# Kernel tuning notes

Hardware: AMD Instinct MI355X
Metric: run time of the kernel (lower is better)

The kernel has to match this reference:

```python
import jax, jax.numpy as jnp
import numpy as np

CAPACITY = 1024


def setup_inputs() -> dict:
    T, H, I, E, K = 2048, 1024, 1408, 8, 2
    key = jax.random.key(0)
    k0, k1, k2, k3, k4 = jax.random.split(key, 5)
    hidden_states = jax.random.normal(k0, (T, H), dtype=jnp.float32)
    w1 = jax.random.normal(k1, (E, 2 * I, H), dtype=jnp.float32) * 0.02  # [gate; up]
    w2 = jax.random.normal(k2, (E, H, I), dtype=jnp.float32) * 0.02
    topk_weights = jax.random.uniform(k3, (T, K), dtype=jnp.float32)
    topk_ids = jax.random.randint(k4, (T, K), 0, E, dtype=jnp.int32)
    return {"hidden_states": hidden_states, "w1": w1, "w2": w2,
            "topk_weights": topk_weights, "topk_ids": topk_ids}


def reference(hidden_states, w1, w2, topk_weights, topk_ids):
    # MoE: prepare(dispatch) -> grouped expert GEMM (silu-gated MLP) -> finalize(combine)
    T, H = hidden_states.shape
    E = w1.shape[0]
    I = w2.shape[2]
    K = topk_ids.shape[1]
    C = CAPACITY

    # ---- prepare: dispatch token copies to per-expert buffers ----
    flat_ids = topk_ids.reshape(-1)                       # (T*K,)
    onehot = jax.nn.one_hot(flat_ids, E, dtype=jnp.int32)  # (T*K, E)
    cs = jnp.cumsum(onehot, axis=0)                        # running per-expert counts
    pos = jnp.take_along_axis(cs, flat_ids[:, None], axis=1)[:, 0] - 1  # slot in expert buffer
    keep = pos < C
    pos_c = jnp.where(keep, pos, 0)

    x_flat = jnp.repeat(hidden_states, K, axis=0)          # (T*K, H)
    x_e = jnp.zeros((E, C, H), dtype=hidden_states.dtype)
    x_e = x_e.at[flat_ids, pos_c].add(jnp.where(keep[:, None], x_flat, 0.0))

    # ---- grouped expert GEMM: silu(gate) * up, then down-proj ----
    h = jnp.einsum('ech,eoh->eco', x_e, w1)                # (E, C, 2I)
    gate, up = h[..., :I], h[..., I:]
    act = jax.nn.silu(gate) * up                           # (E, C, I)
    y = jnp.einsum('eci,ehi->ech', act, w2)                # (E, C, H)

    # ---- finalize: gather back, apply router weights, reduce over top-k ----
    y_flat = y[flat_ids, pos_c] * (keep[:, None].astype(y.dtype)) \
             * topk_weights.reshape(-1, 1)                 # (T*K, H)
    out = y_flat.reshape(T, K, H).sum(axis=1)              # (T, H)
    return out.astype(hidden_states.dtype)
```

## Files before the change

kernel.cpp:

```cpp
#include <hip/hip_runtime.h>

#define NE 8
#define CAP 1024
#define HD 1024
#define ID 1408
#define TT 2048

typedef __attribute__((ext_vector_type(8))) short bf16x8;
typedef __attribute__((ext_vector_type(4))) float f32x4;
typedef unsigned short u16;
typedef unsigned int u32;
typedef unsigned long long u64;

__device__ __forceinline__ u16 f2bf(float f) {
  u32 u = __float_as_uint(f);
  u = (u + 0x7fffu + ((u >> 16) & 1u)) >> 16;
  return (u16)u;
}

__device__ __forceinline__ bf16x8 pack8(float4 a, float4 b) {
  bf16x8 r;
  r[0] = (short)f2bf(a.x); r[1] = (short)f2bf(a.y);
  r[2] = (short)f2bf(a.z); r[3] = (short)f2bf(a.w);
  r[4] = (short)f2bf(b.x); r[5] = (short)f2bf(b.y);
  r[6] = (short)f2bf(b.z); r[7] = (short)f2bf(b.w);
  return r;
}

__device__ __forceinline__ void async_cp16(const void* g, void* l) {
  __builtin_amdgcn_global_load_lds(
      (const __attribute__((address_space(1))) u32*)g,
      (__attribute__((address_space(3))) u32*)l, 16, 0, 0);
}

#define W1B (NE * 2 * ID / 4)
#define W2B (NE * HD * ID / 4096)
#define XB (TT * HD / 4096)
__global__ __launch_bounds__(256) void prep_kernel(
    const float4* __restrict__ w1, bf16x8* __restrict__ bw1,
    const float4* __restrict__ w2, bf16x8* __restrict__ bw2,
    const float4* __restrict__ x, bf16x8* __restrict__ bx,
    float4* __restrict__ out, const int* __restrict__ ids,
    int* __restrict__ rowmap, int* __restrict__ counts) {
  int b = blockIdx.x;
  int tid = threadIdx.x;
  if (b == 0) {
    __shared__ unsigned char ids_s[TT * 2];
    __shared__ int sc[256][NE + 1];
    for (int i = tid; i < TT * 2; i += 256) ids_s[i] = (unsigned char)ids[i];
    __syncthreads();
    int base = tid * 16;
    u64 own64 = 0;
#pragma unroll
    for (int j = 0; j < 16; ++j) own64 += 1ull << (ids_s[base + j] * 8);
    int own[NE];
#pragma unroll
    for (int e = 0; e < NE; ++e) {
      own[e] = (int)((own64 >> (e * 8)) & 0xff);
      sc[tid][e] = own[e];
    }
    __syncthreads();
    for (int off = 1; off < 256; off <<= 1) {
      int v[NE];
      if (tid >= off) {
#pragma unroll
        for (int e = 0; e < NE; ++e) v[e] = sc[tid - off][e];
      }
      __syncthreads();
      if (tid >= off) {
#pragma unroll
        for (int e = 0; e < NE; ++e) sc[tid][e] += v[e];
      }
      __syncthreads();
    }
    if (tid == 255) {
#pragma unroll
      for (int e = 0; e < NE; ++e) counts[e] = sc[255][e] < CAP ? sc[255][e] : CAP;
    }
    int excl[NE];
#pragma unroll
    for (int e = 0; e < NE; ++e) excl[e] = sc[tid][e] - own[e];
    __syncthreads();
#pragma unroll
    for (int e = 0; e < NE; ++e) sc[tid][e] = excl[e];
#pragma unroll
    for (int j = 0; j < 16; ++j) {
      int f = base + j;
      int e = ids_s[f];
      int p = sc[tid][e]++;
      if (p < CAP) rowmap[e * CAP + p] = f;
    }
    return;
  }
  int bb = b - 1;
  if (bb < W1B) {
    int rl = tid >> 6, c = tid & 63;
    int g = bb * 4 + rl;
    int e = g / (2 * ID);
    int n = g - e * (2 * ID);
    int j = (n < ID) ? n : (n - ID);
    int np = (j >> 4) * 32 + (j & 15) + ((n < ID) ? 0 : 16);
    const float4* src = w1 + ((size_t)e * 2 * ID + n) * (HD / 4);
    bf16x8* dst = bw1 + ((size_t)e * 2 * ID + np) * (HD / 8);
    float4 v0 = src[c * 2];
    float4 v1 = src[c * 2 + 1];
    float4 v2 = src[128 + c * 2];
    float4 v3 = src[128 + c * 2 + 1];
    dst[c] = pack8(v0, v1);
    dst[64 + c] = pack8(v2, v3);
  } else if (bb < W1B + W2B) {
    size_t base4 = (size_t)(bb - W1B) * 1024;
    float4 v0 = w2[base4 + tid * 2];
    float4 v1 = w2[base4 + tid * 2 + 1];
    float4 v2 = w2[base4 + 512 + tid * 2];
    float4 v3 = w2[base4 + 512 + tid * 2 + 1];
    bf16x8* dst = bw2 + base4 / 2;
    dst[tid] = pack8(v0, v1);
    dst[256 + tid] = pack8(v2, v3);
  } else {
    size_t base4 = (size_t)(bb - W1B - W2B) * 1024;
    float4 v0 = x[base4 + tid * 2];
    float4 v1 = x[base4 + tid * 2 + 1];
    float4 v2 = x[base4 + 512 + tid * 2];
    float4 v3 = x[base4 + 512 + tid * 2 + 1];
    bf16x8* dst = bx + base4 / 2;
    dst[tid] = pack8(v0, v1);
    dst[256 + tid] = pack8(v2, v3);
    float4 z = {0.f, 0.f, 0.f, 0.f};
    out[base4 + tid] = z;
    out[base4 + 256 + tid] = z;
    out[base4 + 512 + tid] = z;
    out[base4 + 768 + tid] = z;
  }
}

__global__ __launch_bounds__(256) void gemm1_kernel(
    const u16* __restrict__ A, const u16* __restrict__ B, u16* __restrict__ Hb,
    const int* __restrict__ rowmap, const int* __restrict__ counts) {
  int e = blockIdx.x;
  int count = counts[e];
  int m0 = blockIdx.y * 128;
  if (m0 >= count) return;
  int n0 = blockIdx.z * 128;
  int tid = threadIdx.x;
  int lane = tid & 63, wid = tid >> 6;
  int wm = wid >> 1, wn = wid & 1;
  int q = lane >> 4, lm = lane & 15;

  __shared__ __align__(16) char sm[32768];
  char* smA = sm;
  char* smB = sm + 16384;

  int rloc = tid >> 3;
  int chs = ((tid & 7) ^ (rloc & 7)) * 8;
  const u16* aP[4];
  const u16* bP[4];
#pragma unroll
  for (int i = 0; i < 4; ++i) {
    int gr = m0 + rloc + 32 * i;
    int f = (gr < count) ? rowmap[e * CAP + gr] : 0;
    aP[i] = A + (size_t)(f >> 1) * HD + chs;
    bP[i] = B + ((size_t)e * 2 * ID + n0 + rloc + 32 * i) * HD + chs;
  }

  f32x4 zero = {0.f, 0.f, 0.f, 0.f};
  f32x4 acc[4][4];
#pragma unroll
  for (int mi = 0; mi < 4; ++mi)
#pragma unroll
    for (int ni = 0; ni < 4; ++ni) acc[mi][ni] = zero;

  for (int kt = 0; kt < HD / 64; ++kt) {
    int ko = kt * 64;
#pragma unroll
    for (int i = 0; i < 4; ++i)
      async_cp16(aP[i] + ko, smA + (i * 256 + tid) * 16);
#pragma unroll
    for (int i = 0; i < 4; ++i)
      async_cp16(bP[i] + ko, smB + (i * 256 + tid) * 16);
    asm volatile("s_waitcnt vmcnt(0)" ::: "memory");
    __syncthreads();
#pragma unroll
    for (int s = 0; s < 2; ++s) {
      bf16x8 af[4], bfr[4];
#pragma unroll
      for (int mi = 0; mi < 4; ++mi) {
        int row = wm * 64 + mi * 16 + lm;
        af[mi] = *(const bf16x8*)(smA + row * 128 + (((s * 4 + q) ^ (lm & 7)) * 16));
      }
#pragma unroll
      for (int ni = 0; ni < 4; ++ni) {
        int row = wn * 64 + ni * 16 + lm;
        bfr[ni] = *(const bf16x8*)(smB + row * 128 + (((s * 4 + q) ^ (lm & 7)) * 16));
      }
#pragma unroll
      for (int mi = 0; mi < 4; ++mi)
#pragma unroll
        for (int ni = 0; ni < 4; ++ni)
          acc[mi][ni] = __builtin_amdgcn_mfma_f32_16x16x32_bf16(af[mi], bfr[ni], acc[mi][ni], 0, 0, 0);
    }
    __syncthreads();
  }

  u16* smOut = (u16*)sm;
#pragma unroll
  for (int mi = 0; mi < 4; ++mi) {
#pragma unroll
    for (int k = 0; k < 2; ++k) {
      int colL = wn * 32 + k * 16 + lm;
#pragma unroll
      for (int r = 0; r < 4; ++r) {
        float g = acc[mi][2 * k][r];
        float u = acc[mi][2 * k + 1][r];
        float a = g / (1.f + __expf(-g)) * u;
        int row = wm * 64 + mi * 16 + q * 4 + r;
        smOut[row * 72 + colL] = f2bf(a);
      }
    }
  }
  __syncthreads();
  {
    int row = tid >> 1, seg = tid & 1;
    const u16* sp = smOut + row * 72 + seg * 32;
    bf16x8 v0 = *(const bf16x8*)sp;
    bf16x8 v1 = *(const bf16x8*)(sp + 8);
    bf16x8 v2 = *(const bf16x8*)(sp + 16);
    bf16x8 v3 = *(const bf16x8*)(sp + 24);
    u16* dp = Hb + ((size_t)e * CAP + m0 + row) * ID + (n0 >> 1) + seg * 32;
    *(bf16x8*)dp = v0;
    *(bf16x8*)(dp + 8) = v1;
    *(bf16x8*)(dp + 16) = v2;
    *(bf16x8*)(dp + 24) = v3;
  }
}

__global__ __launch_bounds__(256) void gemm2_kernel(
    const u16* __restrict__ A, const u16* __restrict__ B, float* __restrict__ out,
    const int* __restrict__ rowmap, const int* __restrict__ counts,
    const float* __restrict__ tw) {
  int e = blockIdx.x;
  int count = counts[e];
  int m0 = blockIdx.y * 64;
  if (m0 >= count) return;
  int n0 = blockIdx.z * 64;
  int tid = threadIdx.x;
  int lane = tid & 63, wid = tid >> 6;
  int wm = wid >> 1, wn = wid & 1;
  int q = lane >> 4, lm = lane & 15;

  __shared__ __align__(16) char smA[64 * 128];
  __shared__ __align__(16) char smB[64 * 128];

  int rloc = tid >> 3;
  int chs = ((tid & 7) ^ (rloc & 7)) * 8;
  const u16* aP[2];
  const u16* bP[2];
#pragma unroll
  for (int i = 0; i < 2; ++i) {
    aP[i] = A + ((size_t)e * CAP + m0 + rloc + 32 * i) * ID + chs;
    bP[i] = B + ((size_t)e * HD + n0 + rloc + 32 * i) * ID + chs;
  }

  f32x4 zero = {0.f, 0.f, 0.f, 0.f};
  f32x4 acc[2][2];
#pragma unroll
  for (int mi = 0; mi < 2; ++mi)
#pragma unroll
    for (int ni = 0; ni < 2; ++ni) acc[mi][ni] = zero;

  for (int kt = 0; kt < ID / 64; ++kt) {
    int ko = kt * 64;
#pragma unroll
    for (int i = 0; i < 2; ++i) {
      async_cp16(aP[i] + ko, smA + (i * 256 + tid) * 16);
      async_cp16(bP[i] + ko, smB + (i * 256 + tid) * 16);
    }
    asm volatile("s_waitcnt vmcnt(0)" ::: "memory");
    __syncthreads();
#pragma unroll
    for (int s = 0; s < 2; ++s) {
      bf16x8 af[2], bfr[2];
#pragma unroll
      for (int mi = 0; mi < 2; ++mi) {
        int row = wm * 32 + mi * 16 + lm;
        af[mi] = *(const bf16x8*)(smA + row * 128 + (((s * 4 + q) ^ (lm & 7)) * 16));
      }
#pragma unroll
      for (int ni = 0; ni < 2; ++ni) {
        int row = wn * 32 + ni * 16 + lm;
        bfr[ni] = *(const bf16x8*)(smB + row * 128 + (((s * 4 + q) ^ (lm & 7)) * 16));
      }
#pragma unroll
      for (int mi = 0; mi < 2; ++mi)
#pragma unroll
        for (int ni = 0; ni < 2; ++ni)
          acc[mi][ni] = __builtin_amdgcn_mfma_f32_16x16x32_bf16(af[mi], bfr[ni], acc[mi][ni], 0, 0, 0);
    }
    __syncthreads();
  }

#pragma unroll
  for (int mi = 0; mi < 2; ++mi) {
#pragma unroll
    for (int r = 0; r < 4; ++r) {
      int grow = m0 + wm * 32 + mi * 16 + q * 4 + r;
      if (grow < count) {
        int f = rowmap[e * CAP + grow];
        float w = tw[f];
        int t = f >> 1;
#pragma unroll
        for (int ni = 0; ni < 2; ++ni) {
          int col = n0 + wn * 32 + ni * 16 + lm;
          atomicAdd(&out[(size_t)t * HD + col], w * acc[mi][ni][r]);
        }
      }
    }
  }
}

extern "C" void kernel_launch(void* const* d_in, const int* in_sizes, int n_in,
                              void* d_out, int out_size, void* d_ws, size_t ws_size,
                              hipStream_t stream) {
  const float* hidden = (const float*)d_in[0];
  const float* w1 = (const float*)d_in[1];
  const float* w2 = (const float*)d_in[2];
  const float* tw = (const float*)d_in[3];
  const int* ids = (const int*)d_in[4];
  float* out = (float*)d_out;

  char* p = (char*)d_ws;
  auto alloc = [&](size_t b) { char* r = p; p += (b + 255) & ~(size_t)255; return r; };
  u16* bw1 = (u16*)alloc((size_t)NE * 2 * ID * HD * 2);
  u16* bw2 = (u16*)alloc((size_t)NE * HD * ID * 2);
  u16* bx = (u16*)alloc((size_t)TT * HD * 2);
  u16* hbuf = (u16*)alloc((size_t)NE * CAP * ID * 2);
  int* rowmap = (int*)alloc((size_t)NE * CAP * 4);
  int* counts = (int*)alloc((size_t)NE * 4);

  prep_kernel<<<1 + W1B + W2B + XB, 256, 0, stream>>>(
      (const float4*)w1, (bf16x8*)bw1, (const float4*)w2, (bf16x8*)bw2,
      (const float4*)hidden, (bf16x8*)bx, (float4*)out, ids, rowmap, counts);

  gemm1_kernel<<<dim3(NE, CAP / 128, 2 * ID / 128), 256, 0, stream>>>(
      bx, bw1, hbuf, rowmap, counts);

  gemm2_kernel<<<dim3(NE, CAP / 64, HD / 64), 256, 0, stream>>>(
      hbuf, bw2, out, rowmap, counts, tw);
}
```

Baseline: 272.5 us.

## Double-buffer LDS in expert GEMMs, persistent M loop, larger gemm2 tile

Both expert GEMM kernels now double-buffer shared memory, issuing the next K-tile's async copies before computing on the current one. The grid's M dimension is cut to 4 blocks that stride over rows in steps of 512, so fewer blocks exit early. gemm2 grows its tile from 64x64 to 128x64, and the MFMA sections are wrapped in s_setprio. Shared memory per block doubles, which may lower occupancy, and the strided loop can unbalance work when per-expert counts differ.

```diff
diff --git a/kernel.cpp b/kernel.cpp
--- a/kernel.cpp
+++ b/kernel.cpp
@@ -139,98 +139,116 @@
     const int* __restrict__ rowmap, const int* __restrict__ counts) {
   int e = blockIdx.x;
   int count = counts[e];
-  int m0 = blockIdx.y * 128;
-  if (m0 >= count) return;
   int n0 = blockIdx.z * 128;
   int tid = threadIdx.x;
   int lane = tid & 63, wid = tid >> 6;
   int wm = wid >> 1, wn = wid & 1;
   int q = lane >> 4, lm = lane & 15;
 
-  __shared__ __align__(16) char sm[32768];
-  char* smA = sm;
-  char* smB = sm + 16384;
+  __shared__ __align__(16) char sm[2][32768];
 
   int rloc = tid >> 3;
   int chs = ((tid & 7) ^ (rloc & 7)) * 8;
-  const u16* aP[4];
+  int ar = (wm * 64 + lm) * 128;
+  int br = 16384 + (wn * 64 + lm) * 128;
+  int cs0 = (q ^ (lm & 7)) * 16;
+  int cs1 = ((4 + q) ^ (lm & 7)) * 16;
+
   const u16* bP[4];
 #pragma unroll
-  for (int i = 0; i < 4; ++i) {
-    int gr = m0 + rloc + 32 * i;
-    int f = (gr < count) ? rowmap[e * CAP + gr] : 0;
-    aP[i] = A + (size_t)(f >> 1) * HD + chs;
+  for (int i = 0; i < 4; ++i)
     bP[i] = B + ((size_t)e * 2 * ID + n0 + rloc + 32 * i) * HD + chs;
-  }
-
-  f32x4 zero = {0.f, 0.f, 0.f, 0.f};
-  f32x4 acc[4][4];
-#pragma unroll
-  for (int mi = 0; mi < 4; ++mi)
-#pragma unroll
-    for (int ni = 0; ni < 4; ++ni) acc[mi][ni] = zero;
-
-  for (int kt = 0; kt < HD / 64; ++kt) {
-    int ko = kt * 64;
-#pragma unroll
-    for (int i = 0; i < 4; ++i)
-      async_cp16(aP[i] + ko, smA + (i * 256 + tid) * 16);
-#pragma unroll
-    for (int i = 0; i < 4; ++i)
-      async_cp16(bP[i] + ko, smB + (i * 256 + tid) * 16);
+
+  for (int m0 = blockIdx.y * 128; m0 < count; m0 += 512) {
+    const u16* aP[4];
+#pragma unroll
+    for (int i = 0; i < 4; ++i) {
+      int gr = m0 + rloc + 32 * i;
+      int f = (gr < count) ? rowmap[e * CAP + gr] : 0;
+      aP[i] = A + (size_t)(f >> 1) * HD + chs;
+    }
+
+    f32x4 zero = {0.f, 0.f, 0.f, 0.f};
+    f32x4 acc[4][4];
+#pragma unroll
+    for (int mi = 0; mi < 4; ++mi)
+#pragma unroll
+      for (int ni = 0; ni < 4; ++ni) acc[mi][ni] = zero;
+
+#define STAGE1(buf, kt)                                                    \
+  do {                                                                     \
+    int ko_ = (kt) * 64;                                                   \
+    async_cp16(aP[0] + ko_, sm[buf] + (0 * 256 + tid) * 16);               \
+    async_cp16(aP[1] + ko_, sm[buf] + (1 * 256 + tid) * 16);               \
+    async_cp16(aP[2] + ko_, sm[buf] + (2 * 256 + tid) * 16);               \
+    async_cp16(aP[3] + ko_, sm[buf] + (3 * 256 + tid) * 16);               \
+    async_cp16(bP[0] + ko_, sm[buf] + 16384 + (0 * 256 + tid) * 16);       \
+    async_cp16(bP[1] + ko_, sm[buf] + 16384 + (1 * 256 + tid) * 16);       \
+    async_cp16(bP[2] + ko_, sm[buf] + 16384 + (2 * 256 + tid) * 16);       \
+    async_cp16(bP[3] + ko_, sm[buf] + 16384 + (3 * 256 + tid) * 16);       \
+  } while (0)
+
+    STAGE1(0, 0);
     asm volatile("s_waitcnt vmcnt(0)" ::: "memory");
     __syncthreads();
-#pragma unroll
-    for (int s = 0; s < 2; ++s) {
-      bf16x8 af[4], bfr[4];
-#pragma unroll
-      for (int mi = 0; mi < 4; ++mi) {
-        int row = wm * 64 + mi * 16 + lm;
-        af[mi] = *(const bf16x8*)(smA + row * 128 + (((s * 4 + q) ^ (lm & 7)) * 16));
-      }
-#pragma unroll
-      for (int ni = 0; ni < 4; ++ni) {
-        int row = wn * 64 + ni * 16 + lm;
-        bfr[ni] = *(const bf16x8*)(smB + row * 128 + (((s * 4 + q) ^ (lm & 7)) * 16));
-      }
-#pragma unroll
-      for (int mi = 0; mi < 4; ++mi)
+    int cur = 0;
+    for (int kt = 0; kt < HD / 64; ++kt) {
+      if (kt < HD / 64 - 1) STAGE1(cur ^ 1, kt + 1);
+      const char* sb = sm[cur];
+#pragma unroll
+      for (int s = 0; s < 2; ++s) {
+        int cs = s ? cs1 : cs0;
+        bf16x8 af[4], bfr[4];
+#pragma unroll
+        for (int mi = 0; mi < 4; ++mi)
+          af[mi] = *(const bf16x8*)(sb + ar + mi * 2048 + cs);
 #pragma unroll
         for (int ni = 0; ni < 4; ++ni)
-          acc[mi][ni] = __builtin_amdgcn_mfma_f32_16x16x32_bf16(af[mi], bfr[ni], acc[mi][ni], 0, 0, 0);
-    }
-    __syncthreads();
-  }
-
-  u16* smOut = (u16*)sm;
-#pragma unroll
-  for (int mi = 0; mi < 4; ++mi) {
-#pragma unroll
-    for (int k = 0; k < 2; ++k) {
-      int colL = wn * 32 + k * 16 + lm;
-#pragma unroll
-      for (int r = 0; r < 4; ++r) {
-        float g = acc[mi][2 * k][r];
-        float u = acc[mi][2 * k + 1][r];
-        float a = g / (1.f + __expf(-g)) * u;
-        int row = wm * 64 + mi * 16 + q * 4 + r;
-        smOut[row * 72 + colL] = f2bf(a);
-      }
-    }
-  }
-  __syncthreads();
-  {
-    int row = tid >> 1, seg = tid & 1;
-    const u16* sp = smOut + row * 72 + seg * 32;
-    bf16x8 v0 = *(const bf16x8*)sp;
-    bf16x8 v1 = *(const bf16x8*)(sp + 8);
-    bf16x8 v2 = *(const bf16x8*)(sp + 16);
-    bf16x8 v3 = *(const bf16x8*)(sp + 24);
-    u16* dp = Hb + ((size_t)e * CAP + m0 + row) * ID + (n0 >> 1) + seg * 32;
-    *(bf16x8*)dp = v0;
-    *(bf16x8*)(dp + 8) = v1;
-    *(bf16x8*)(dp + 16) = v2;
-    *(bf16x8*)(dp + 24) = v3;
+          bfr[ni] = *(const bf16x8*)(sb + br + ni * 2048 + cs);
+        __builtin_amdgcn_s_setprio(1);
+#pragma unroll
+        for (int mi = 0; mi < 4; ++mi)
+#pragma unroll
+          for (int ni = 0; ni < 4; ++ni)
+            acc[mi][ni] = __builtin_amdgcn_mfma_f32_16x16x32_bf16(af[mi], bfr[ni], acc[mi][ni], 0, 0, 0);
+        __builtin_amdgcn_s_setprio(0);
+      }
+      asm volatile("s_waitcnt vmcnt(0)" ::: "memory");
+      __syncthreads();
+      cur ^= 1;
+    }
+
+    u16* smOut = (u16*)sm;
+#pragma unroll
+    for (int mi = 0; mi < 4; ++mi) {
+#pragma unroll
+      for (int k = 0; k < 2; ++k) {
+        int colL = wn * 32 + k * 16 + lm;
+#pragma unroll
+        for (int r = 0; r < 4; ++r) {
+          float g = acc[mi][2 * k][r];
+          float u = acc[mi][2 * k + 1][r];
+          float a = g / (1.f + __expf(-g)) * u;
+          int row = wm * 64 + mi * 16 + q * 4 + r;
+          smOut[row * 72 + colL] = f2bf(a);
+        }
+      }
+    }
+    __syncthreads();
+    {
+      int row = tid >> 1, seg = tid & 1;
+      const u16* sp = smOut + row * 72 + seg * 32;
+      bf16x8 v0 = *(const bf16x8*)sp;
+      bf16x8 v1 = *(const bf16x8*)(sp + 8);
+      bf16x8 v2 = *(const bf16x8*)(sp + 16);
+      bf16x8 v3 = *(const bf16x8*)(sp + 24);
+      u16* dp = Hb + ((size_t)e * CAP + m0 + row) * ID + (n0 >> 1) + seg * 32;
+      *(bf16x8*)dp = v0;
+      *(bf16x8*)(dp + 8) = v1;
+      *(bf16x8*)(dp + 16) = v2;
+      *(bf16x8*)(dp + 24) = v3;
+    }
+    __syncthreads();
   }
 }
 
@@ -240,78 +258,94 @@
     const float* __restrict__ tw) {
   int e = blockIdx.x;
   int count = counts[e];
-  int m0 = blockIdx.y * 64;
-  if (m0 >= count) return;
   int n0 = blockIdx.z * 64;
   int tid = threadIdx.x;
   int lane = tid & 63, wid = tid >> 6;
   int wm = wid >> 1, wn = wid & 1;
   int q = lane >> 4, lm = lane & 15;
 
-  __shared__ __align__(16) char smA[64 * 128];
-  __shared__ __align__(16) char smB[64 * 128];
+  __shared__ __align__(16) char sm[2][24576];
 
   int rloc = tid >> 3;
   int chs = ((tid & 7) ^ (rloc & 7)) * 8;
-  const u16* aP[2];
+  int ar = (wm * 64 + lm) * 128;
+  int br = 16384 + (wn * 32 + lm) * 128;
+  int cs0 = (q ^ (lm & 7)) * 16;
+  int cs1 = ((4 + q) ^ (lm & 7)) * 16;
+
   const u16* bP[2];
 #pragma unroll
-  for (int i = 0; i < 2; ++i) {
-    aP[i] = A + ((size_t)e * CAP + m0 + rloc + 32 * i) * ID + chs;
+  for (int i = 0; i < 2; ++i)
     bP[i] = B + ((size_t)e * HD + n0 + rloc + 32 * i) * ID + chs;
-  }
-
-  f32x4 zero = {0.f, 0.f, 0.f, 0.f};
-  f32x4 acc[2][2];
-#pragma unroll
-  for (int mi = 0; mi < 2; ++mi)
-#pragma unroll
-    for (int ni = 0; ni < 2; ++ni) acc[mi][ni] = zero;
-
-  for (int kt = 0; kt < ID / 64; ++kt) {
-    int ko = kt * 64;
-#pragma unroll
-    for (int i = 0; i < 2; ++i) {
-      async_cp16(aP[i] + ko, smA + (i * 256 + tid) * 16);
-      async_cp16(bP[i] + ko, smB + (i * 256 + tid) * 16);
-    }
+
+  for (int m0 = blockIdx.y * 128; m0 < count; m0 += 512) {
+    const u16* aP[4];
+#pragma unroll
+    for (int i = 0; i < 4; ++i)
+      aP[i] = A + ((size_t)e * CAP + m0 + rloc + 32 * i) * ID + chs;
+
+    f32x4 zero = {0.f, 0.f, 0.f, 0.f};
+    f32x4 acc[4][2];
+#pragma unroll
+    for (int mi = 0; mi < 4; ++mi)
+#pragma unroll
+      for (int ni = 0; ni < 2; ++ni) acc[mi][ni] = zero;
+
+#define STAGE2(buf, kt)                                                    \
+  do {                                                                     \
+    int ko_ = (kt) * 64;                                                   \
+    async_cp16(aP[0] + ko_, sm[buf] + (0 * 256 + tid) * 16);               \
+    async_cp16(aP[1] + ko_, sm[buf] + (1 * 256 + tid) * 16);               \
+    async_cp16(aP[2] + ko_, sm[buf] + (2 * 256 + tid) * 16);               \
+    async_cp16(aP[3] + ko_, sm[buf] + (3 * 256 + tid) * 16);               \
+    async_cp16(bP[0] + ko_, sm[buf] + 16384 + (0 * 256 + tid) * 16);       \
+    async_cp16(bP[1] + ko_, sm[buf] + 16384 + (1 * 256 + tid) * 16);       \
+  } while (0)
+
+    STAGE2(0, 0);
     asm volatile("s_waitcnt vmcnt(0)" ::: "memory");
     __syncthreads();
-#pragma unroll
-    for (int s = 0; s < 2; ++s) {
-      bf16x8 af[2], bfr[2];
-#pragma unroll
-      for (int mi = 0; mi < 2; ++mi) {
-        int row = wm * 32 + mi * 16 + lm;
-        af[mi] = *(const bf16x8*)(smA + row * 128 + (((s * 4 + q) ^ (lm & 7)) * 16));
-      }
-#pragma unroll
-      for (int ni = 0; ni < 2; ++ni) {
-        int row = wn * 32 + ni * 16 + lm;
-        bfr[ni] = *(const bf16x8*)(smB + row * 128 + (((s * 4 + q) ^ (lm & 7)) * 16));
-      }
-#pragma unroll
-      for (int mi = 0; mi < 2; ++mi)
+    int cur = 0;
+    for (int kt = 0; kt < ID / 64; ++kt) {
+      if (kt < ID / 64 - 1) STAGE2(cur ^ 1, kt + 1);
+      const char* sb = sm[cur];
+#pragma unroll
+      for (int s = 0; s < 2; ++s) {
+        int cs = s ? cs1 : cs0;
+        bf16x8 af[4], bfr[2];
+#pragma unroll
+        for (int mi = 0; mi < 4; ++mi)
+          af[mi] = *(const bf16x8*)(sb + ar + mi * 2048 + cs);
 #pragma unroll
         for (int ni = 0; ni < 2; ++ni)
-          acc[mi][ni] = __builtin_amdgcn_mfma_f32_16x16x32_bf16(af[mi], bfr[ni], acc[mi][ni], 0, 0, 0);
-    }
-    __syncthreads();
-  }
-
-#pragma unroll
-  for (int mi = 0; mi < 2; ++mi) {
-#pragma unroll
-    for (int r = 0; r < 4; ++r) {
-      int grow = m0 + wm * 32 + mi * 16 + q * 4 + r;
-      if (grow < count) {
-        int f = rowmap[e * CAP + grow];
-        float w = tw[f];
-        int t = f >> 1;
-#pragma unroll
-        for (int ni = 0; ni < 2; ++ni) {
-          int col = n0 + wn * 32 + ni * 16 + lm;
-          atomicAdd(&out[(size_t)t * HD + col], w * acc[mi][ni][r]);
+          bfr[ni] = *(const bf16x8*)(sb + br + ni * 2048 + cs);
+        __builtin_amdgcn_s_setprio(1);
+#pragma unroll
+        for (int mi = 0; mi < 4; ++mi)
+#pragma unroll
+          for (int ni = 0; ni < 2; ++ni)
+            acc[mi][ni] = __builtin_amdgcn_mfma_f32_16x16x32_bf16(af[mi], bfr[ni], acc[mi][ni], 0, 0, 0);
+        __builtin_amdgcn_s_setprio(0);
+      }
+      asm volatile("s_waitcnt vmcnt(0)" ::: "memory");
+      __syncthreads();
+      cur ^= 1;
+    }
+
+#pragma unroll
+    for (int mi = 0; mi < 4; ++mi) {
+#pragma unroll
+      for (int r = 0; r < 4; ++r) {
+        int grow = m0 + wm * 64 + mi * 16 + q * 4 + r;
+        if (grow < count) {
+          int f = rowmap[e * CAP + grow];
+          float w = tw[f];
+          int t = f >> 1;
+#pragma unroll
+          for (int ni = 0; ni < 2; ++ni) {
+            int col = n0 + wn * 32 + ni * 16 + lm;
+            atomicAdd(&out[(size_t)t * HD + col], w * acc[mi][ni][r]);
+          }
         }
       }
     }
@@ -341,9 +375,9 @@
       (const float4*)w1, (bf16x8*)bw1, (const float4*)w2, (bf16x8*)bw2,
       (const float4*)hidden, (bf16x8*)bx, (float4*)out, ids, rowmap, counts);
 
-  gemm1_kernel<<<dim3(NE, CAP / 128, 2 * ID / 128), 256, 0, stream>>>(
+  gemm1_kernel<<<dim3(NE, 4, 2 * ID / 128), 256, 0, stream>>>(
       bx, bw1, hbuf, rowmap, counts);
 
-  gemm2_kernel<<<dim3(NE, CAP / 64, HD / 64), 256, 0, stream>>>(
+  gemm2_kernel<<<dim3(NE, 4, HD / 64), 256, 0, stream>>>(
       hbuf, bw2, out, rowmap, counts, tw);
 }
```

Result: slower. 296.7 us (+8.9%).

## Triple-buffer async loads in both expert GEMMs and halve gemm1 M tile

Applied to the files above, without the earlier changes.

Both GEMM kernels now keep three shared-memory stages, prefetching two k-tiles ahead and waiting with partial vmcnt counts, so global-to-LDS copies overlap the MFMA work instead of stalling on every iteration. gemm1's M tile shrinks from 128 to 64 rows, which doubles the grid and reduces wasted work on partially filled expert buffers. MFMA sections are wrapped in s_setprio. The trade-off is more LDS per block (72KB in gemm1), which may limit occupancy, and less B-tile reuse in gemm1.

```diff
diff --git a/kernel.cpp b/kernel.cpp
--- a/kernel.cpp
+++ b/kernel.cpp
@@ -134,12 +134,13 @@
   }
 }
 
+#define G1BUF 24576
 __global__ __launch_bounds__(256) void gemm1_kernel(
     const u16* __restrict__ A, const u16* __restrict__ B, u16* __restrict__ Hb,
     const int* __restrict__ rowmap, const int* __restrict__ counts) {
   int e = blockIdx.x;
   int count = counts[e];
-  int m0 = blockIdx.y * 128;
+  int m0 = blockIdx.y * 64;
   if (m0 >= count) return;
   int n0 = blockIdx.z * 128;
   int tid = threadIdx.x;
@@ -147,64 +148,77 @@
   int wm = wid >> 1, wn = wid & 1;
   int q = lane >> 4, lm = lane & 15;
 
-  __shared__ __align__(16) char sm[32768];
-  char* smA = sm;
-  char* smB = sm + 16384;
+  __shared__ __align__(16) char sm[3 * G1BUF];
 
   int rloc = tid >> 3;
   int chs = ((tid & 7) ^ (rloc & 7)) * 8;
-  const u16* aP[4];
+  const u16* aP[2];
   const u16* bP[4];
 #pragma unroll
-  for (int i = 0; i < 4; ++i) {
+  for (int i = 0; i < 2; ++i) {
     int gr = m0 + rloc + 32 * i;
     int f = (gr < count) ? rowmap[e * CAP + gr] : 0;
     aP[i] = A + (size_t)(f >> 1) * HD + chs;
+  }
+#pragma unroll
+  for (int i = 0; i < 4; ++i)
     bP[i] = B + ((size_t)e * 2 * ID + n0 + rloc + 32 * i) * HD + chs;
-  }
 
   f32x4 zero = {0.f, 0.f, 0.f, 0.f};
-  f32x4 acc[4][4];
-#pragma unroll
-  for (int mi = 0; mi < 4; ++mi)
+  f32x4 acc[2][4];
+#pragma unroll
+  for (int mi = 0; mi < 2; ++mi)
 #pragma unroll
     for (int ni = 0; ni < 4; ++ni) acc[mi][ni] = zero;
 
+#define STAGE1(base, kt)                                             \
+  do {                                                               \
+    int ko_ = (kt) * 64;                                             \
+    char* sb_ = (base);                                              \
+    async_cp16(aP[0] + ko_, sb_ + (0 * 256 + tid) * 16);             \
+    async_cp16(aP[1] + ko_, sb_ + (1 * 256 + tid) * 16);             \
+    async_cp16(bP[0] + ko_, sb_ + 8192 + (0 * 256 + tid) * 16);      \
+    async_cp16(bP[1] + ko_, sb_ + 8192 + (1 * 256 + tid) * 16);      \
+    async_cp16(bP[2] + ko_, sb_ + 8192 + (2 * 256 + tid) * 16);      \
+    async_cp16(bP[3] + ko_, sb_ + 8192 + (3 * 256 + tid) * 16);      \
+  } while (0)
+
+  STAGE1(sm, 0);
+  STAGE1(sm + G1BUF, 1);
+  int p = 0, pn2 = 2;
   for (int kt = 0; kt < HD / 64; ++kt) {
-    int ko = kt * 64;
-#pragma unroll
-    for (int i = 0; i < 4; ++i)
-      async_cp16(aP[i] + ko, smA + (i * 256 + tid) * 16);
-#pragma unroll
-    for (int i = 0; i < 4; ++i)
-      async_cp16(bP[i] + ko, smB + (i * 256 + tid) * 16);
-    asm volatile("s_waitcnt vmcnt(0)" ::: "memory");
-    __syncthreads();
+    if (kt == HD / 64 - 1)
+      asm volatile("s_waitcnt vmcnt(0)\ns_barrier" ::: "memory");
+    else
+      asm volatile("s_waitcnt vmcnt(6)\ns_barrier" ::: "memory");
+    const char* sb = sm + p * G1BUF;
+    if (kt + 2 < HD / 64) STAGE1(sm + pn2 * G1BUF, kt + 2);
 #pragma unroll
     for (int s = 0; s < 2; ++s) {
-      bf16x8 af[4], bfr[4];
-#pragma unroll
-      for (int mi = 0; mi < 4; ++mi) {
-        int row = wm * 64 + mi * 16 + lm;
-        af[mi] = *(const bf16x8*)(smA + row * 128 + (((s * 4 + q) ^ (lm & 7)) * 16));
-      }
-#pragma unroll
-      for (int ni = 0; ni < 4; ++ni) {
-        int row = wn * 64 + ni * 16 + lm;
-        bfr[ni] = *(const bf16x8*)(smB + row * 128 + (((s * 4 + q) ^ (lm & 7)) * 16));
-      }
-#pragma unroll
-      for (int mi = 0; mi < 4; ++mi)
+      int cs = ((s * 4 + q) ^ (lm & 7)) * 16;
+      bf16x8 af[2], bfr[4];
+#pragma unroll
+      for (int mi = 0; mi < 2; ++mi)
+        af[mi] = *(const bf16x8*)(sb + (wm * 32 + mi * 16 + lm) * 128 + cs);
+#pragma unroll
+      for (int ni = 0; ni < 4; ++ni)
+        bfr[ni] = *(const bf16x8*)(sb + 8192 + (wn * 64 + ni * 16 + lm) * 128 + cs);
+      __builtin_amdgcn_s_setprio(1);
+#pragma unroll
+      for (int mi = 0; mi < 2; ++mi)
 #pragma unroll
         for (int ni = 0; ni < 4; ++ni)
           acc[mi][ni] = __builtin_amdgcn_mfma_f32_16x16x32_bf16(af[mi], bfr[ni], acc[mi][ni], 0, 0, 0);
-    }
-    __syncthreads();
-  }
+      __builtin_amdgcn_s_setprio(0);
+    }
+    p = (p == 2) ? 0 : p + 1;
+    pn2 = (pn2 == 2) ? 0 : pn2 + 1;
+  }
+  __syncthreads();
 
   u16* smOut = (u16*)sm;
 #pragma unroll
-  for (int mi = 0; mi < 4; ++mi) {
+  for (int mi = 0; mi < 2; ++mi) {
 #pragma unroll
     for (int k = 0; k < 2; ++k) {
       int colL = wn * 32 + k * 16 + lm;
@@ -213,27 +227,24 @@
         float g = acc[mi][2 * k][r];
         float u = acc[mi][2 * k + 1][r];
         float a = g / (1.f + __expf(-g)) * u;
-        int row = wm * 64 + mi * 16 + q * 4 + r;
+        int row = wm * 32 + mi * 16 + q * 4 + r;
         smOut[row * 72 + colL] = f2bf(a);
       }
     }
   }
   __syncthreads();
   {
-    int row = tid >> 1, seg = tid & 1;
-    const u16* sp = smOut + row * 72 + seg * 32;
+    int row = tid >> 2, seg = tid & 3;
+    const u16* sp = smOut + row * 72 + seg * 16;
     bf16x8 v0 = *(const bf16x8*)sp;
     bf16x8 v1 = *(const bf16x8*)(sp + 8);
-    bf16x8 v2 = *(const bf16x8*)(sp + 16);
-    bf16x8 v3 = *(const bf16x8*)(sp + 24);
-    u16* dp = Hb + ((size_t)e * CAP + m0 + row) * ID + (n0 >> 1) + seg * 32;
+    u16* dp = Hb + ((size_t)e * CAP + m0 + row) * ID + (n0 >> 1) + seg * 16;
     *(bf16x8*)dp = v0;
     *(bf16x8*)(dp + 8) = v1;
-    *(bf16x8*)(dp + 16) = v2;
-    *(bf16x8*)(dp + 24) = v3;
-  }
-}
-
+  }
+}
+
+#define G2BUF 16384
 __global__ __launch_bounds__(256) void gemm2_kernel(
     const u16* __restrict__ A, const u16* __restrict__ B, float* __restrict__ out,
     const int* __restrict__ rowmap, const int* __restrict__ counts,
@@ -248,8 +259,7 @@
   int wm = wid >> 1, wn = wid & 1;
   int q = lane >> 4, lm = lane & 15;
 
-  __shared__ __align__(16) char smA[64 * 128];
-  __shared__ __align__(16) char smB[64 * 128];
+  __shared__ __align__(16) char sm[3 * G2BUF];
 
   int rloc = tid >> 3;
   int chs = ((tid & 7) ^ (rloc & 7)) * 8;
@@ -268,35 +278,46 @@
 #pragma unroll
     for (int ni = 0; ni < 2; ++ni) acc[mi][ni] = zero;
 
+#define STAGE2(base, kt)                                             \
+  do {                                                               \
+    int ko_ = (kt) * 64;                                             \
+    char* sb_ = (base);                                              \
+    async_cp16(aP[0] + ko_, sb_ + (0 * 256 + tid) * 16);             \
+    async_cp16(aP[1] + ko_, sb_ + (1 * 256 + tid) * 16);             \
+    async_cp16(bP[0] + ko_, sb_ + 8192 + (0 * 256 + tid) * 16);      \
+    async_cp16(bP[1] + ko_, sb_ + 8192 + (1 * 256 + tid) * 16);      \
+  } while (0)
+
+  STAGE2(sm, 0);
+  STAGE2(sm + G2BUF, 1);
+  int p = 0, pn2 = 2;
   for (int kt = 0; kt < ID / 64; ++kt) {
-    int ko = kt * 64;
-#pragma unroll
-    for (int i = 0; i < 2; ++i) {
-      async_cp16(aP[i] + ko, smA + (i * 256 + tid) * 16);
-      async_cp16(bP[i] + ko, smB + (i * 256 + tid) * 16);
-    }
-    asm volatile("s_waitcnt vmcnt(0)" ::: "memory");
-    __syncthreads();
+    if (kt == ID / 64 - 1)
+      asm volatile("s_waitcnt vmcnt(0)\ns_barrier" ::: "memory");
+    else
+      asm volatile("s_waitcnt vmcnt(4)\ns_barrier" ::: "memory");
+    const char* sb = sm + p * G2BUF;
+    if (kt + 2 < ID / 64) STAGE2(sm + pn2 * G2BUF, kt + 2);
 #pragma unroll
     for (int s = 0; s < 2; ++s) {
+      int cs = ((s * 4 + q) ^ (lm & 7)) * 16;
       bf16x8 af[2], bfr[2];
 #pragma unroll
-      for (int mi = 0; mi < 2; ++mi) {
-        int row = wm * 32 + mi * 16 + lm;
-        af[mi] = *(const bf16x8*)(smA + row * 128 + (((s * 4 + q) ^ (lm & 7)) * 16));
-      }
-#pragma unroll
-      for (int ni = 0; ni < 2; ++ni) {
-        int row = wn * 32 + ni * 16 + lm;
-        bfr[ni] = *(const bf16x8*)(smB + row * 128 + (((s * 4 + q) ^ (lm & 7)) * 16));
-      }
+      for (int mi = 0; mi < 2; ++mi)
+        af[mi] = *(const bf16x8*)(sb + (wm * 32 + mi * 16 + lm) * 128 + cs);
+#pragma unroll
+      for (int ni = 0; ni < 2; ++ni)
+        bfr[ni] = *(const bf16x8*)(sb + 8192 + (wn * 32 + ni * 16 + lm) * 128 + cs);
+      __builtin_amdgcn_s_setprio(1);
 #pragma unroll
       for (int mi = 0; mi < 2; ++mi)
 #pragma unroll
         for (int ni = 0; ni < 2; ++ni)
           acc[mi][ni] = __builtin_amdgcn_mfma_f32_16x16x32_bf16(af[mi], bfr[ni], acc[mi][ni], 0, 0, 0);
-    }
-    __syncthreads();
+      __builtin_amdgcn_s_setprio(0);
+    }
+    p = (p == 2) ? 0 : p + 1;
+    pn2 = (pn2 == 2) ? 0 : pn2 + 1;
   }
 
 #pragma unroll
@@ -341,7 +362,7 @@
       (const float4*)w1, (bf16x8*)bw1, (const float4*)w2, (bf16x8*)bw2,
       (const float4*)hidden, (bf16x8*)bx, (float4*)out, ids, rowmap, counts);
 
-  gemm1_kernel<<<dim3(NE, CAP / 128, 2 * ID / 128), 256, 0, stream>>>(
+  gemm1_kernel<<<dim3(NE, CAP / 64, 2 * ID / 128), 256, 0, stream>>>(
       bx, bw1, hbuf, rowmap, counts);
 
   gemm2_kernel<<<dim3(NE, CAP / 64, HD / 64), 256, 0, stream>>>(
```

New measurement: 262.3 us. 3.8% less time.
